# Optimization experiments

Hardware: AMD Instinct MI355X
Metric: run time of the kernel (lower is better)

## Reference

```python
import jax, jax.numpy as jnp
import numpy as np

HEADS = 8
NEG_SLOPE = 0.2  # PyG GATConv default LeakyReLU slope


def _gat_layer(x, src, dst, W, a_src, a_dst, bias, heads, out_ch):
    """PyG-style GATConv (concat heads, self-loops already appended, eval mode).
    x: [N, F_in]; src/dst: [E_tot] int; W: [F_in, heads*out_ch];
    a_src/a_dst: [heads, out_ch]; bias: [heads*out_ch].
    """
    N = x.shape[0]
    h = (x @ W).reshape(N, heads, out_ch)                      # [N, H, C]
    # per-node attention logits (gathered per edge as scalars, not features)
    al_s = jnp.einsum('nhc,hc->nh', h, a_src)                  # [N, H]
    al_d = jnp.einsum('nhc,hc->nh', h, a_dst)                  # [N, H]
    e = jax.nn.leaky_relu(al_s[src] + al_d[dst], negative_slope=NEG_SLOPE)  # [E, H]
    # segment softmax over incoming edges of each target node (stable)
    e_max = jax.ops.segment_max(e, dst, num_segments=N)        # self-loops => no empty segments
    ex = jnp.exp(e - e_max[dst])
    denom = jax.ops.segment_sum(ex, dst, num_segments=N)
    alpha = ex / (denom[dst] + 1e-16)                          # [E, H]
    # gather source features, weight, scatter-add to targets
    out = jax.ops.segment_sum(h[src] * alpha[:, :, None], dst, num_segments=N)  # [N, H, C]
    return out.reshape(N, heads * out_ch) + bias


def setup_inputs() -> dict:
    key = jax.random.key(0)
    ks = jax.random.split(key, 16)
    N, E, F_IN, NUM_CLASSES = 50000, 1600000, 128, 16
    s = 0.1
    return {
        'x': jax.random.normal(ks[0], (N, F_IN), dtype=jnp.float32),
        'edge_index': jax.random.randint(ks[1], (2, E), 0, N, dtype=jnp.int64),
        # GAT layer 1: 128 -> 8 heads x 8
        'W1': jax.random.normal(ks[2], (F_IN, 64), dtype=jnp.float32) * s,
        'a1_src': jax.random.normal(ks[3], (8, 8), dtype=jnp.float32) * s,
        'a1_dst': jax.random.normal(ks[4], (8, 8), dtype=jnp.float32) * s,
        'b1': jnp.zeros((64,), dtype=jnp.float32),
        # GAT layer 2: 64 -> 8 heads x 4
        'W2': jax.random.normal(ks[5], (64, 32), dtype=jnp.float32) * s,
        'a2_src': jax.random.normal(ks[6], (8, 4), dtype=jnp.float32) * s,
        'a2_dst': jax.random.normal(ks[7], (8, 4), dtype=jnp.float32) * s,
        'b2': jnp.zeros((32,), dtype=jnp.float32),
        # torch MultiheadAttention(32, 8): packed in_proj [96,32], out_proj [32,32]
        'in_proj_w': jax.random.normal(ks[8], (96, 32), dtype=jnp.float32) * s,
        'in_proj_b': jnp.zeros((96,), dtype=jnp.float32),
        'out_proj_w': jax.random.normal(ks[9], (32, 32), dtype=jnp.float32) * s,
        'out_proj_b': jnp.zeros((32,), dtype=jnp.float32),
        # fc: 32 -> num_classes
        'fc_w': jax.random.normal(ks[10], (NUM_CLASSES, 32), dtype=jnp.float32) * s,
        'fc_b': jnp.zeros((NUM_CLASSES,), dtype=jnp.float32),
    }


def reference(x, edge_index, W1, a1_src, a1_dst, b1, W2, a2_src, a2_dst, b2,
              in_proj_w, in_proj_b, out_proj_w, out_proj_b, fc_w, fc_b):
    N = x.shape[0]
    loops = jnp.arange(N, dtype=edge_index.dtype)
    src = jnp.concatenate([edge_index[0], loops])  # PyG add_self_loops=True
    dst = jnp.concatenate([edge_index[1], loops])

    h = jax.nn.elu(_gat_layer(x, src, dst, W1, a1_src, a1_dst, b1, HEADS, 8))   # [N, 64]
    h = jax.nn.elu(_gat_layer(h, src, dst, W2, a2_src, a2_dst, b2, HEADS, 4))   # [N, 32]

    # MultiheadAttention on h.unsqueeze(0): shape [1, N, 32] with torch's
    # seq-first layout => seq_len = 1, batch = N. Softmax over a single key
    # is identically 1 for every head, so out = out_proj(v_proj(h)).
    v = h @ in_proj_w[64:96].T + in_proj_b[64:96]   # v-projection slice of packed in_proj
    h = v @ out_proj_w.T + out_proj_b               # [N, 32]

    logits = h @ fc_w.T + fc_b                      # [N, num_classes]
    return jax.nn.log_softmax(logits, axis=1)
```

## Files before the change

### kernel.cpp

```cpp
#include <hip/hip_runtime.h>
#include <hip/hip_bf16.h>
#include <math.h>


#define BSHIFT 7
#define BMASK  ((1 << BSHIFT) - 1)
#define MAXNB  512
#define TILE   8192
#define XST    136
#define SMBYTES 36864
#define LESRC_MAX 6144

typedef __attribute__((ext_vector_type(8))) short short8;
typedef __attribute__((ext_vector_type(4))) float floatx4;
typedef __attribute__((ext_vector_type(2))) float floatx2;

__device__ __forceinline__ unsigned short f2bf(float f) {
    union { float f; unsigned int u; } v; v.f = f;
    unsigned int u = v.u;
    return (unsigned short)((u + 0x7FFFu + ((u >> 16) & 1u)) >> 16);
}
__device__ __forceinline__ float lrelu(float e) { return fmaxf(e, 0.2f * e); }
__device__ __forceinline__ float elu(float o) {
    return (o > 0.f) ? o : (__expf(o) - 1.f);
}

__global__ __launch_bounds__(256) void fused_pre_kernel(
    const float* __restrict__ x, const float* __restrict__ W,
    const float* __restrict__ a_src, const float* __restrict__ a_dst,
    char* __restrict__ rec1, float* __restrict__ ald, int N, int GB,
    const int* __restrict__ ei, int E, int Et, int NB, int CAP,
    int* __restrict__ gcount, unsigned int* __restrict__ rec, int NT,
    const float* __restrict__ in_proj_w, const float* __restrict__ in_proj_b,
    const float* __restrict__ out_proj_w, const float* __restrict__ out_proj_b,
    const float* __restrict__ fc_w, const float* __restrict__ fc_b,
    float* __restrict__ M, float* __restrict__ bf) {
    __shared__ __align__(16) char sm[SMBYTES];
    int t = threadIdx.x;
    int bid = blockIdx.x;
    if (bid < GB) {
        unsigned short* xs = (unsigned short*)sm;
        unsigned short* wt = xs + 64 * XST;
        int nb = bid * 64;
#pragma unroll
        for (int r = 0; r < 8; ++r) {
            int p = t + 256 * r;
            int row = p >> 5;
            int c4  = p & 31;
            int n = nb + row;
            float4 v = (n < N) ? ((const float4*)x)[(size_t)n * 32 + c4]
                               : make_float4(0.f, 0.f, 0.f, 0.f);
            unsigned short* dst = &xs[row * XST + c4 * 4];
            dst[0] = f2bf(v.x); dst[1] = f2bf(v.y);
            dst[2] = f2bf(v.z); dst[3] = f2bf(v.w);
        }
        {
            int n = t & 63, kg = t >> 6;
#pragma unroll
            for (int c = 0; c < 4; ++c) {
                int k0 = kg * 32 + c * 8;
                unsigned short* dst = &wt[n * XST + k0];
#pragma unroll
                for (int j = 0; j < 8; ++j)
                    dst[j] = f2bf(W[(k0 + j) * 64 + n]);
            }
        }
        __syncthreads();
        int wave = t >> 6, lane = t & 63;
        int m16 = lane & 15, quad = lane >> 4;
        floatx4 acc[4];
#pragma unroll
        for (int i = 0; i < 4; ++i) acc[i] = (floatx4){0.f, 0.f, 0.f, 0.f};
#pragma unroll
        for (int k = 0; k < 4; ++k) {
            int koff = k * 32 + quad * 8;
            short8 afrag = *(const short8*)&xs[(wave * 16 + m16) * XST + koff];
#pragma unroll
            for (int nt = 0; nt < 4; ++nt) {
                short8 bfrag = *(const short8*)&wt[(nt * 16 + m16) * XST + koff];
                acc[nt] = __builtin_amdgcn_mfma_f32_16x16x32_bf16(afrag, bfrag, acc[nt], 0, 0, 0);
            }
        }
        __syncthreads();
        float* hs = (float*)sm;
#pragma unroll
        for (int nt = 0; nt < 4; ++nt)
#pragma unroll
            for (int r = 0; r < 4; ++r)
                hs[(wave * 16 + quad * 4 + r) * 65 + nt * 16 + m16] = acc[nt][r];
        __syncthreads();
        float asv = a_src[lane], adv = a_dst[lane];
        for (int itn = 0; itn < 16; ++itn) {
            int nl = wave * 16 + itn;
            int n = nb + nl;
            if (n >= N) break;
            float v = hs[nl * 65 + lane];
            float ps = v * asv, pd = v * adv;
            ps += __shfl_xor(ps, 1); ps += __shfl_xor(ps, 2); ps += __shfl_xor(ps, 4);
            pd += __shfl_xor(pd, 1); pd += __shfl_xor(pd, 2); pd += __shfl_xor(pd, 4);
            if ((lane & 7) == 0) {
                *(float*)(rec1 + (size_t)n * 128 + 4 * (lane >> 3)) = ps;
                ald[n * 8 + (lane >> 3)] = pd;
            }
            if (lane < 16) {
                const float* hr = &hs[nl * 65 + lane * 4];
                int pk = __builtin_amdgcn_cvt_pk_fp8_f32(hr[0], hr[1], 0, false);
                pk = __builtin_amdgcn_cvt_pk_fp8_f32(hr[2], hr[3], pk, true);
                *(unsigned*)(rec1 + (size_t)n * 128 + 64 + 4 * lane) = (unsigned)pk;
            }
        }
    } else if (bid < GB + NT) {
        unsigned int* lrec = (unsigned int*)sm;
        int* h   = (int*)(sm + TILE * 4);
        int* cur = (int*)(sm + TILE * 4 + MAXNB * 4);
        for (int i = t; i < NB; i += 256) h[i] = 0;
        int tile0 = (bid - GB) * TILE;
        int cnt = Et - tile0; if (cnt > TILE) cnt = TILE;
        __syncthreads();
        for (int j = t; j < cnt; j += 256) {
            int jj = tile0 + j;
            int srcv, d;
            if (jj < E) { srcv = ei[jj]; d = ei[E + jj]; } else { srcv = jj - E; d = jj - E; }
            lrec[j] = (unsigned)srcv | ((unsigned)d << 16);
            atomicAdd(&h[d >> BSHIFT], 1);
        }
        __syncthreads();
        for (int i = t; i < NB; i += 256)
            cur[i] = h[i] ? atomicAdd(&gcount[i], h[i]) : 0;
        __syncthreads();
        for (int j = t; j < cnt; j += 256) {
            unsigned v = lrec[j];
            int b = v >> (16 + BSHIFT);
            int pos = atomicAdd(&cur[b], 1);
            if (pos < CAP)
                rec[(size_t)b * CAP + pos] =
                    (v & 0xFFFFu) | ((((v >> 16) & BMASK)) << 16);
        }
    } else {
        float* Wvo = (float*)sm;
        float* bvo = (float*)(sm + 4096);
        const float* Wv = in_proj_w + 64 * 32;
        const float* bv = in_proj_b + 64;
        for (int idx = t; idx < 1024; idx += 256) {
            int i = idx >> 5, j = idx & 31;
            float acc = 0.f;
            for (int k = 0; k < 32; ++k) acc += out_proj_w[i * 32 + k] * Wv[k * 32 + j];
            Wvo[idx] = acc;
        }
        if (t < 32) {
            float acc = 0.f;
            for (int k = 0; k < 32; ++k) acc += out_proj_w[t * 32 + k] * bv[k];
            bvo[t] = acc + out_proj_b[t];
        }
        __syncthreads();
        for (int idx = t; idx < 16 * 32; idx += 256) {
            int cc = idx >> 5, j = idx & 31;
            float acc = 0.f;
            for (int i = 0; i < 32; ++i) acc += fc_w[cc * 32 + i] * Wvo[i * 32 + j];
            M[idx] = acc;
        }
        if (t < 16) {
            float acc = 0.f;
            for (int i = 0; i < 32; ++i) acc += fc_w[t * 32 + i] * bvo[i];
            bf[t] = acc + fc_b[t];
        }
    }
}

__global__ __launch_bounds__(256) void csr_finalize_kernel(
    const unsigned int* __restrict__ rec, const int* __restrict__ gcount,
    int* __restrict__ rowp, unsigned short* __restrict__ esrc,
    int N, int Et, int CAP) {
    __shared__ int h[128];
    __shared__ int nb[128];
    __shared__ int cur[128];
    __shared__ int ssum[256];
    __shared__ unsigned short lesrc[LESRC_MAX];
    int b = blockIdx.x, t = threadIdx.x;
    size_t rbase = (size_t)b * CAP;
    int cnt = gcount[b]; if (cnt > CAP) cnt = CAP;
    if (t < 128) h[t] = 0;
    int acc = 0;
    for (int i = t; i < b; i += 256) {
        int v = gcount[i];
        acc += (v < CAP) ? v : CAP;
    }
    ssum[t] = acc;
    __syncthreads();
    for (int off = 128; off >= 1; off >>= 1) {
        if (t < off) ssum[t] += ssum[t + off];
        __syncthreads();
    }
    int obase = ssum[0];
    for (int i = t; i < cnt; i += 256)
        atomicAdd(&h[(rec[rbase + i] >> 16) & 127], 1);
    __syncthreads();
    if (t == 0) {
        int run = 0;
        for (int i = 0; i < 128; ++i) { nb[i] = run; run += h[i]; }
    }
    __syncthreads();
    if (t < 128) cur[t] = nb[t];
    int n0 = b << BSHIFT;
    if (t < 128 && n0 + t < N) rowp[n0 + t] = obase + nb[t];
    if (b == 0 && t == 0) rowp[N] = Et;
    __syncthreads();
    for (int i = t; i < cnt; i += 256) {
        unsigned r = rec[rbase + i];
        int pos = atomicAdd(&cur[(r >> 16) & 127], 1);
        lesrc[pos] = (unsigned short)(r & 0xFFFFu);
    }
    __syncthreads();
    for (int i = t; i < cnt; i += 256)
        esrc[obase + i] = lesrc[i];
}

__global__ __launch_bounds__(256) void gat_agg64_g2_kernel(
    const int* __restrict__ rowp, const unsigned short* __restrict__ esrc,
    const char* __restrict__ rec1, const float* __restrict__ ald_arr,
    const float* __restrict__ bias,
    const float* __restrict__ W2, const float* __restrict__ a2s,
    const float* __restrict__ a2d,
    char* __restrict__ rec2, float* __restrict__ ald2, int N) {
    __shared__ __align__(16) float W2p[2][8][32][4];
    __shared__ __align__(16) float oL[4][64];
    __shared__ __align__(16) float h2L[4][32];
    int t = threadIdx.x;
    for (int idx = t; idx < 2048; idx += 256) {
        int k = idx >> 5, l = idx & 31;
        W2p[k >> 5][(k & 31) >> 2][l][k & 3] = W2[idx];
    }
    __syncthreads();
    const int lane = t & 63;
    const int wv = t >> 6;
    const int e = lane >> 3;
    const int c = lane & 7;
    const int aoff = 4 * c;
    const int foff = 64 + 8 * c;
    int n = blockIdx.x * 4 + wv;
    if (n >= N) return;
    float aldv = ald_arr[n * 8 + c];
    int beg = rowp[n], end = rowp[n + 1];
    float dA = 0.f, dB = 0.f;
    floatx2 A0 = {0.f, 0.f}, A1 = {0.f, 0.f}, A2 = {0.f, 0.f}, A3 = {0.f, 0.f};
    floatx2 B0 = {0.f, 0.f}, B1 = {0.f, 0.f}, B2 = {0.f, 0.f}, B3 = {0.f, 0.f};
    int i = beg;
    for (; i + 32 <= end; i += 32) {
        int s0 = esrc[i + e],      s1 = esrc[i + 8 + e];
        int s2 = esrc[i + 16 + e], s3 = esrc[i + 24 + e];
        const char* r0 = rec1 + (size_t)s0 * 128;
        const char* r1 = rec1 + (size_t)s1 * 128;
        const char* r2 = rec1 + (size_t)s2 * 128;
        const char* r3 = rec1 + (size_t)s3 * 128;
        float e0 = *(const float*)(r0 + aoff), e1 = *(const float*)(r1 + aoff);
        float e2 = *(const float*)(r2 + aoff), e3 = *(const float*)(r3 + aoff);
        uint2 g0 = *(const uint2*)(r0 + foff), g1 = *(const uint2*)(r1 + foff);
        uint2 g2 = *(const uint2*)(r2 + foff), g3 = *(const uint2*)(r3 + foff);
        float w0 = __expf(lrelu(e0 + aldv));
        float w1 = __expf(lrelu(e1 + aldv));
        float w2 = __expf(lrelu(e2 + aldv));
        float w3 = __expf(lrelu(e3 + aldv));
        dA += w0 + w2; dB += w1 + w3;
        A0 += w0 * __builtin_amdgcn_cvt_pk_f32_fp8(g0.x, false);
        A1 += w0 * __builtin_amdgcn_cvt_pk_f32_fp8(g0.x, true);
        A2 += w0 * __builtin_amdgcn_cvt_pk_f32_fp8(g0.y, false);
        A3 += w0 * __builtin_amdgcn_cvt_pk_f32_fp8(g0.y, true);
        B0 += w1 * __builtin_amdgcn_cvt_pk_f32_fp8(g1.x, false);
        B1 += w1 * __builtin_amdgcn_cvt_pk_f32_fp8(g1.x, true);
        B2 += w1 * __builtin_amdgcn_cvt_pk_f32_fp8(g1.y, false);
        B3 += w1 * __builtin_amdgcn_cvt_pk_f32_fp8(g1.y, true);
        A0 += w2 * __builtin_amdgcn_cvt_pk_f32_fp8(g2.x, false);
        A1 += w2 * __builtin_amdgcn_cvt_pk_f32_fp8(g2.x, true);
        A2 += w2 * __builtin_amdgcn_cvt_pk_f32_fp8(g2.y, false);
        A3 += w2 * __builtin_amdgcn_cvt_pk_f32_fp8(g2.y, true);
        B0 += w3 * __builtin_amdgcn_cvt_pk_f32_fp8(g3.x, false);
        B1 += w3 * __builtin_amdgcn_cvt_pk_f32_fp8(g3.x, true);
        B2 += w3 * __builtin_amdgcn_cvt_pk_f32_fp8(g3.y, false);
        B3 += w3 * __builtin_amdgcn_cvt_pk_f32_fp8(g3.y, true);
    }
    for (; i < end; i += 32) {
        int i0 = i + e, i1 = i + 8 + e, i2 = i + 16 + e, i3 = i + 24 + e;
        bool v0 = i0 < end, v1 = i1 < end, v2 = i2 < end, v3 = i3 < end;
        int c0 = v0 ? i0 : beg;
        int c1 = v1 ? i1 : beg;
        int c2 = v2 ? i2 : beg;
        int c3 = v3 ? i3 : beg;
        int s0 = esrc[c0], s1 = esrc[c1], s2 = esrc[c2], s3 = esrc[c3];
        const char* r0 = rec1 + (size_t)s0 * 128;
        const char* r1 = rec1 + (size_t)s1 * 128;
        const char* r2 = rec1 + (size_t)s2 * 128;
        const char* r3 = rec1 + (size_t)s3 * 128;
        float e0 = *(const float*)(r0 + aoff), e1 = *(const float*)(r1 + aoff);
        float e2 = *(const float*)(r2 + aoff), e3 = *(const float*)(r3 + aoff);
        uint2 g0 = *(const uint2*)(r0 + foff), g1 = *(const uint2*)(r1 + foff);
        uint2 g2 = *(const uint2*)(r2 + foff), g3 = *(const uint2*)(r3 + foff);
        float w0 = v0 ? __expf(lrelu(e0 + aldv)) : 0.f;
        float w1 = v1 ? __expf(lrelu(e1 + aldv)) : 0.f;
        float w2 = v2 ? __expf(lrelu(e2 + aldv)) : 0.f;
        float w3 = v3 ? __expf(lrelu(e3 + aldv)) : 0.f;
        dA += w0 + w2; dB += w1 + w3;
        A0 += w0 * __builtin_amdgcn_cvt_pk_f32_fp8(g0.x, false);
        A1 += w0 * __builtin_amdgcn_cvt_pk_f32_fp8(g0.x, true);
        A2 += w0 * __builtin_amdgcn_cvt_pk_f32_fp8(g0.y, false);
        A3 += w0 * __builtin_amdgcn_cvt_pk_f32_fp8(g0.y, true);
        B0 += w1 * __builtin_amdgcn_cvt_pk_f32_fp8(g1.x, false);
        B1 += w1 * __builtin_amdgcn_cvt_pk_f32_fp8(g1.x, true);
        B2 += w1 * __builtin_amdgcn_cvt_pk_f32_fp8(g1.y, false);
        B3 += w1 * __builtin_amdgcn_cvt_pk_f32_fp8(g1.y, true);
        A0 += w2 * __builtin_amdgcn_cvt_pk_f32_fp8(g2.x, false);
        A1 += w2 * __builtin_amdgcn_cvt_pk_f32_fp8(g2.x, true);
        A2 += w2 * __builtin_amdgcn_cvt_pk_f32_fp8(g2.y, false);
        A3 += w2 * __builtin_amdgcn_cvt_pk_f32_fp8(g2.y, true);
        B0 += w3 * __builtin_amdgcn_cvt_pk_f32_fp8(g3.x, false);
        B1 += w3 * __builtin_amdgcn_cvt_pk_f32_fp8(g3.x, true);
        B2 += w3 * __builtin_amdgcn_cvt_pk_f32_fp8(g3.y, false);
        B3 += w3 * __builtin_amdgcn_cvt_pk_f32_fp8(g3.y, true);
    }
    float d = dA + dB;
    float P0 = A0.x + B0.x, P1 = A0.y + B0.y;
    float P2 = A1.x + B1.x, P3 = A1.y + B1.y;
    float P4 = A2.x + B2.x, P5 = A2.y + B2.y;
    float P6 = A3.x + B3.x, P7 = A3.y + B3.y;
    d  += __shfl_xor(d, 8);  d  += __shfl_xor(d, 16);  d  += __shfl_xor(d, 32);
    P0 += __shfl_xor(P0, 8); P0 += __shfl_xor(P0, 16); P0 += __shfl_xor(P0, 32);
    P1 += __shfl_xor(P1, 8); P1 += __shfl_xor(P1, 16); P1 += __shfl_xor(P1, 32);
    P2 += __shfl_xor(P2, 8); P2 += __shfl_xor(P2, 16); P2 += __shfl_xor(P2, 32);
    P3 += __shfl_xor(P3, 8); P3 += __shfl_xor(P3, 16); P3 += __shfl_xor(P3, 32);
    P4 += __shfl_xor(P4, 8); P4 += __shfl_xor(P4, 16); P4 += __shfl_xor(P4, 32);
    P5 += __shfl_xor(P5, 8); P5 += __shfl_xor(P5, 16); P5 += __shfl_xor(P5, 32);
    P6 += __shfl_xor(P6, 8); P6 += __shfl_xor(P6, 16); P6 += __shfl_xor(P6, 32);
    P7 += __shfl_xor(P7, 8); P7 += __shfl_xor(P7, 16); P7 += __shfl_xor(P7, 32);
    float inv = 1.f / (d + 1e-16f);
    float4 bv0 = ((const float4*)bias)[2 * c];
    float4 bv1 = ((const float4*)bias)[2 * c + 1];
    float o0 = elu(P0 * inv + bv0.x);
    float o1 = elu(P1 * inv + bv0.y);
    float o2 = elu(P2 * inv + bv0.z);
    float o3 = elu(P3 * inv + bv0.w);
    float o4 = elu(P4 * inv + bv1.x);
    float o5 = elu(P5 * inv + bv1.y);
    float o6 = elu(P6 * inv + bv1.z);
    float o7 = elu(P7 * inv + bv1.w);
    if (lane < 8) {
        *(float4*)&oL[wv][c * 8]     = make_float4(o0, o1, o2, o3);
        *(float4*)&oL[wv][c * 8 + 4] = make_float4(o4, o5, o6, o7);
    }
    const int l = lane & 31, kh = lane >> 5;
    const float* orow = &oL[wv][kh * 32];
    float a0 = 0.f, a1 = 0.f, a2 = 0.f, a3 = 0.f;
#pragma unroll
    for (int g = 0; g < 8; ++g) {
        float4 ov = *(const float4*)&orow[g * 4];
        float4 wv4 = *(const float4*)&W2p[kh][g][l][0];
        a0 += ov.x * wv4.x; a1 += ov.y * wv4.y;
        a2 += ov.z * wv4.z; a3 += ov.w * wv4.w;
    }
    float acc = (a0 + a1) + (a2 + a3);
    acc += __shfl_xor(acc, 32);
    float ps = acc * a2s[l], pd = acc * a2d[l];
    ps += __shfl_xor(ps, 1); ps += __shfl_xor(ps, 2);
    pd += __shfl_xor(pd, 1); pd += __shfl_xor(pd, 2);
    if (lane < 32) {
        h2L[wv][l] = acc;
        if ((l & 3) == 0) {
            *(float*)(rec2 + (size_t)n * 64 + 4 * (l >> 2)) = ps;
            ald2[n * 8 + (l >> 2)] = pd;
        }
    }
    if (lane < 8) {
        const float* hr = &h2L[wv][lane * 4];
        int pk = __builtin_amdgcn_cvt_pk_fp8_f32(hr[0], hr[1], 0, false);
        pk = __builtin_amdgcn_cvt_pk_fp8_f32(hr[2], hr[3], pk, true);
        *(unsigned*)(rec2 + (size_t)n * 64 + 32 + 4 * lane) = (unsigned)pk;
    }
}

__global__ __launch_bounds__(256) void gat_agg32_fin_kernel(
    const int* __restrict__ rowp, const unsigned short* __restrict__ esrc,
    const char* __restrict__ rec2, const float* __restrict__ ald_arr,
    const float* __restrict__ bias,
    const float* __restrict__ M, const float* __restrict__ bf,
    float* __restrict__ out, int N) {
    __shared__ __align__(16) float Mp[8][16][4];
    __shared__ float bfs[16];
    __shared__ __align__(16) float oL[4][32];
    int t = threadIdx.x;
    for (int i = t; i < 512; i += 256) {
        int j = i >> 5, k = i & 31;
        Mp[k >> 2][j][k & 3] = M[i];
    }
    if (t < 16) bfs[t] = bf[t];
    __syncthreads();
    const int lane = t & 63;
    const int wv = t >> 6;
    const int e = lane >> 3;
    const int c = lane & 7;
    const int aoff = 4 * c;
    const int foff = 32 + 4 * c;
    int n = blockIdx.x * 4 + wv;
    if (n >= N) return;
    float aldv = ald_arr[n * 8 + c];
    int beg = rowp[n], end = rowp[n + 1];
    float d0 = 0.f, d1 = 0.f, d2 = 0.f, d3 = 0.f;
    floatx2 p0a = {0.f, 0.f}, p0b = {0.f, 0.f};
    floatx2 p1a = {0.f, 0.f}, p1b = {0.f, 0.f};
    floatx2 p2a = {0.f, 0.f}, p2b = {0.f, 0.f};
    floatx2 p3a = {0.f, 0.f}, p3b = {0.f, 0.f};
    int base = beg;
    for (; base + 32 <= end; base += 32) {
        int s0 = esrc[base + e],      s1 = esrc[base + 8 + e];
        int s2 = esrc[base + 16 + e], s3 = esrc[base + 24 + e];
        const char* r0 = rec2 + (size_t)s0 * 64;
        const char* r1 = rec2 + (size_t)s1 * 64;
        const char* r2 = rec2 + (size_t)s2 * 64;
        const char* r3 = rec2 + (size_t)s3 * 64;
        float e0 = *(const float*)(r0 + aoff) + aldv;
        float e1 = *(const float*)(r1 + aoff) + aldv;
        float e2 = *(const float*)(r2 + aoff) + aldv;
        float e3 = *(const float*)(r3 + aoff) + aldv;
        unsigned g0 = *(const unsigned*)(r0 + foff);
        unsigned g1 = *(const unsigned*)(r1 + foff);
        unsigned g2 = *(const unsigned*)(r2 + foff);
        unsigned g3 = *(const unsigned*)(r3 + foff);
        float w0 = __expf(lrelu(e0));
        float w1 = __expf(lrelu(e1));
        float w2 = __expf(lrelu(e2));
        float w3 = __expf(lrelu(e3));
        d0 += w0; d1 += w1; d2 += w2; d3 += w3;
        p0a += w0 * __builtin_amdgcn_cvt_pk_f32_fp8(g0, false);
        p0b += w0 * __builtin_amdgcn_cvt_pk_f32_fp8(g0, true);
        p1a += w1 * __builtin_amdgcn_cvt_pk_f32_fp8(g1, false);
        p1b += w1 * __builtin_amdgcn_cvt_pk_f32_fp8(g1, true);
        p2a += w2 * __builtin_amdgcn_cvt_pk_f32_fp8(g2, false);
        p2b += w2 * __builtin_amdgcn_cvt_pk_f32_fp8(g2, true);
        p3a += w3 * __builtin_amdgcn_cvt_pk_f32_fp8(g3, false);
        p3b += w3 * __builtin_amdgcn_cvt_pk_f32_fp8(g3, true);
    }
    for (; base < end; base += 32) {
        int i0 = base + e;
        int i1 = base + 8 + e;
        int i2 = base + 16 + e;
        int i3 = base + 24 + e;
        bool v0 = i0 < end, v1 = i1 < end, v2 = i2 < end, v3 = i3 < end;
        int c0 = v0 ? i0 : beg;
        int c1 = v1 ? i1 : beg;
        int c2 = v2 ? i2 : beg;
        int c3 = v3 ? i3 : beg;
        int s0 = esrc[c0], s1 = esrc[c1], s2 = esrc[c2], s3 = esrc[c3];
        const char* r0 = rec2 + (size_t)s0 * 64;
        const char* r1 = rec2 + (size_t)s1 * 64;
        const char* r2 = rec2 + (size_t)s2 * 64;
        const char* r3 = rec2 + (size_t)s3 * 64;
        float e0 = *(const float*)(r0 + aoff) + aldv;
        float e1 = *(const float*)(r1 + aoff) + aldv;
        float e2 = *(const float*)(r2 + aoff) + aldv;
        float e3 = *(const float*)(r3 + aoff) + aldv;
        unsigned g0 = *(const unsigned*)(r0 + foff);
        unsigned g1 = *(const unsigned*)(r1 + foff);
        unsigned g2 = *(const unsigned*)(r2 + foff);
        unsigned g3 = *(const unsigned*)(r3 + foff);
        float w0 = v0 ? __expf(lrelu(e0)) : 0.f;
        float w1 = v1 ? __expf(lrelu(e1)) : 0.f;
        float w2 = v2 ? __expf(lrelu(e2)) : 0.f;
        float w3 = v3 ? __expf(lrelu(e3)) : 0.f;
        d0 += w0; d1 += w1; d2 += w2; d3 += w3;
        p0a += w0 * __builtin_amdgcn_cvt_pk_f32_fp8(g0, false);
        p0b += w0 * __builtin_amdgcn_cvt_pk_f32_fp8(g0, true);
        p1a += w1 * __builtin_amdgcn_cvt_pk_f32_fp8(g1, false);
        p1b += w1 * __builtin_amdgcn_cvt_pk_f32_fp8(g1, true);
        p2a += w2 * __builtin_amdgcn_cvt_pk_f32_fp8(g2, false);
        p2b += w2 * __builtin_amdgcn_cvt_pk_f32_fp8(g2, true);
        p3a += w3 * __builtin_amdgcn_cvt_pk_f32_fp8(g3, false);
        p3b += w3 * __builtin_amdgcn_cvt_pk_f32_fp8(g3, true);
    }
    float d = (d0 + d1) + (d2 + d3);
    floatx2 Pa = (p0a + p1a) + (p2a + p3a);
    floatx2 Pb = (p0b + p1b) + (p2b + p3b);
    float P0 = Pa.x, P1 = Pa.y, P2 = Pb.x, P3 = Pb.y;
    d  += __shfl_xor(d, 8);  d  += __shfl_xor(d, 16);  d  += __shfl_xor(d, 32);
    P0 += __shfl_xor(P0, 8); P0 += __shfl_xor(P0, 16); P0 += __shfl_xor(P0, 32);
    P1 += __shfl_xor(P1, 8); P1 += __shfl_xor(P1, 16); P1 += __shfl_xor(P1, 32);
    P2 += __shfl_xor(P2, 8); P2 += __shfl_xor(P2, 16); P2 += __shfl_xor(P2, 32);
    P3 += __shfl_xor(P3, 8); P3 += __shfl_xor(P3, 16); P3 += __shfl_xor(P3, 32);
    float inv = 1.f / (d + 1e-16f);
    float4 bv = ((const float4*)bias)[c];
    float o0 = elu(P0 * inv + bv.x);
    float o1 = elu(P1 * inv + bv.y);
    float o2 = elu(P2 * inv + bv.z);
    float o3 = elu(P3 * inv + bv.w);
    if (lane < 8) *(float4*)&oL[wv][c * 4] = make_float4(o0, o1, o2, o3);
    const int j = lane & 15;
    const float* orow = oL[wv];
    float a0 = 0.f, a1 = 0.f, a2 = 0.f, a3 = 0.f;
#pragma unroll
    for (int g = 0; g < 8; ++g) {
        float4 ov = *(const float4*)&orow[g * 4];
        float4 mv = *(const float4*)&Mp[g][j][0];
        a0 += ov.x * mv.x; a1 += ov.y * mv.y;
        a2 += ov.z * mv.z; a3 += ov.w * mv.w;
    }
    float logit = (a0 + a1) + (a2 + a3) + bfs[j];
    float mx = logit;
    mx = fmaxf(mx, __shfl_xor(mx, 1));
    mx = fmaxf(mx, __shfl_xor(mx, 2));
    mx = fmaxf(mx, __shfl_xor(mx, 4));
    mx = fmaxf(mx, __shfl_xor(mx, 8));
    float ex = __expf(logit - mx);
    float se = ex;
    se += __shfl_xor(se, 1);
    se += __shfl_xor(se, 2);
    se += __shfl_xor(se, 4);
    se += __shfl_xor(se, 8);
    float res = logit - (mx + __logf(se));
    if (lane < 16) out[(size_t)n * 16 + j] = res;
}

extern "C" void kernel_launch(void* const* d_in, const int* in_sizes, int n_in,
                              void* d_out, int out_size, void* d_ws, size_t ws_size,
                              hipStream_t stream) {
    const float* x   = (const float*)d_in[0];
    const int*   ei  = (const int*)d_in[1];
    const float* W1  = (const float*)d_in[2];
    const float* a1s = (const float*)d_in[3];
    const float* a1d = (const float*)d_in[4];
    const float* b1  = (const float*)d_in[5];
    const float* W2  = (const float*)d_in[6];
    const float* a2s = (const float*)d_in[7];
    const float* a2d = (const float*)d_in[8];
    const float* b2  = (const float*)d_in[9];
    const float* ipw = (const float*)d_in[10];
    const float* ipb = (const float*)d_in[11];
    const float* opw = (const float*)d_in[12];
    const float* opb = (const float*)d_in[13];
    const float* fcw = (const float*)d_in[14];
    const float* fcb = (const float*)d_in[15];
    float* out = (float*)d_out;

    int N = in_sizes[0] / 128;
    int E = in_sizes[1] / 2;
    int Et = E + N;
    int NB = (N + BMASK) >> BSHIFT;
    int NTILES = (Et + TILE - 1) / TILE;
    int GB = (N + 63) / 64;
    int CAP = Et / NB;
    CAP = CAP + CAP / 8 + 256;
    CAP = (CAP + 255) & ~255;
    if (CAP > LESRC_MAX) CAP = LESRC_MAX;

    char* ws = (char*)d_ws;
    size_t off = 0;
    auto alloc = [&](size_t bytes) -> void* {
        void* p = ws + off;
        off += bytes;
        off = (off + 255) & ~(size_t)255;
        return p;
    };
    int*   bcount = (int*)alloc(MAXNB * 4);
    unsigned int*   rec  = (unsigned int*)alloc((size_t)NB * CAP * 4);
    int*   rowp   = (int*)alloc((size_t)(N + 1) * 4);
    unsigned short* esrc = (unsigned short*)alloc((size_t)Et * 2);
    char* rec1   = (char*)alloc((size_t)N * 128);
    float* al1d  = (float*)alloc((size_t)N * 8 * 4);
    char* rec2   = (char*)alloc((size_t)N * 64);
    float* al2d  = (float*)alloc((size_t)N * 8 * 4);
    float* Mf    = (float*)alloc(512 * 4);
    float* bff   = (float*)alloc(16 * 4);
    (void)ws_size; (void)n_in; (void)out_size;

    hipMemsetAsync(bcount, 0, MAXNB * 4, stream);
    fused_pre_kernel<<<GB + NTILES + 1, 256, 0, stream>>>(
        x, W1, a1s, a1d, rec1, al1d, N, GB,
        ei, E, Et, NB, CAP, bcount, rec, NTILES,
        ipw, ipb, opw, opb, fcw, fcb, Mf, bff);
    csr_finalize_kernel<<<NB, 256, 0, stream>>>(rec, bcount, rowp, esrc, N, Et, CAP);

    gat_agg64_g2_kernel<<<(N + 3) / 4, 256, 0, stream>>>(
        rowp, esrc, rec1, al1d, b1, W2, a2s, a2d, rec2, al2d, N);
    gat_agg32_fin_kernel<<<(N + 3) / 4, 256, 0, stream>>>(
        rowp, esrc, rec2, al2d, b2, Mf, bff, out, N);
}
```

Baseline: 212.3 us.

## Compact gather records with fp16 logits, add low-degree fast path, precompute bf16 W

```diff
diff --git a/kernel.cpp b/kernel.cpp
--- a/kernel.cpp
+++ b/kernel.cpp
@@ -1,5 +1,6 @@
 #include <hip/hip_runtime.h>
 #include <hip/hip_bf16.h>
+#include <hip/hip_fp16.h>
 #include <math.h>
 
 
@@ -25,8 +26,18 @@
     return (o > 0.f) ? o : (__expf(o) - 1.f);
 }
 
+__global__ __launch_bounds__(256) void prep_kernel(
+    const float* __restrict__ W, unsigned short* __restrict__ wtb,
+    int* __restrict__ gcount) {
+    int t = threadIdx.x;
+    if (blockIdx.x == 0) { gcount[t] = 0; gcount[t + 256] = 0; }
+    int idx = blockIdx.x * 256 + t;
+    int n = idx >> 7, k = idx & 127;
+    wtb[idx] = f2bf(W[k * 64 + n]);
+}
+
 __global__ __launch_bounds__(256) void fused_pre_kernel(
-    const float* __restrict__ x, const float* __restrict__ W,
+    const float* __restrict__ x, const unsigned short* __restrict__ wtb,
     const float* __restrict__ a_src, const float* __restrict__ a_dst,
     char* __restrict__ rec1, float* __restrict__ ald, int N, int GB,
     const int* __restrict__ ei, int E, int Et, int NB, int CAP,
@@ -59,10 +70,7 @@
 #pragma unroll
             for (int c = 0; c < 4; ++c) {
                 int k0 = kg * 32 + c * 8;
-                unsigned short* dst = &wt[n * XST + k0];
-#pragma unroll
-                for (int j = 0; j < 8; ++j)
-                    dst[j] = f2bf(W[(k0 + j) * 64 + n]);
+                *(short8*)&wt[n * XST + k0] = *(const short8*)&wtb[n * 128 + k0];
             }
         }
         __syncthreads();
@@ -98,15 +106,20 @@
             float ps = v * asv, pd = v * adv;
             ps += __shfl_xor(ps, 1); ps += __shfl_xor(ps, 2); ps += __shfl_xor(ps, 4);
             pd += __shfl_xor(pd, 1); pd += __shfl_xor(pd, 2); pd += __shfl_xor(pd, 4);
-            if ((lane & 7) == 0) {
-                *(float*)(rec1 + (size_t)n * 128 + 4 * (lane >> 3)) = ps;
+            float av = __shfl(ps, (lane & 7) * 8);
+            if ((lane & 7) == 0)
                 ald[n * 8 + (lane >> 3)] = pd;
-            }
-            if (lane < 16) {
-                const float* hr = &hs[nl * 65 + lane * 4];
-                int pk = __builtin_amdgcn_cvt_pk_fp8_f32(hr[0], hr[1], 0, false);
-                pk = __builtin_amdgcn_cvt_pk_fp8_f32(hr[2], hr[3], pk, true);
-                *(unsigned*)(rec1 + (size_t)n * 128 + 64 + 4 * lane) = (unsigned)pk;
+            if (lane < 8) {
+                const float* hr = &hs[nl * 65 + lane * 8];
+                int pk0 = __builtin_amdgcn_cvt_pk_fp8_f32(hr[0], hr[1], 0, false);
+                pk0 = __builtin_amdgcn_cvt_pk_fp8_f32(hr[2], hr[3], pk0, true);
+                int pk1 = __builtin_amdgcn_cvt_pk_fp8_f32(hr[4], hr[5], 0, false);
+                pk1 = __builtin_amdgcn_cvt_pk_fp8_f32(hr[6], hr[7], pk1, true);
+                *(__half*)(rec1 + (size_t)n * 80 + 2 * lane) = __float2half(av);
+                uint2 w2v;
+                w2v.x = (unsigned)pk0;
+                w2v.y = (unsigned)pk1;
+                *(uint2*)(rec1 + (size_t)n * 80 + 16 + 8 * lane) = w2v;
             }
         }
     } else if (bid < GB + NT) {
@@ -226,125 +239,172 @@
     __shared__ __align__(16) float oL[4][64];
     __shared__ __align__(16) float h2L[4][32];
     int t = threadIdx.x;
-    for (int idx = t; idx < 2048; idx += 256) {
-        int k = idx >> 5, l = idx & 31;
-        W2p[k >> 5][(k & 31) >> 2][l][k & 3] = W2[idx];
-    }
-    __syncthreads();
     const int lane = t & 63;
     const int wv = t >> 6;
     const int e = lane >> 3;
     const int c = lane & 7;
-    const int aoff = 4 * c;
-    const int foff = 64 + 8 * c;
+    const int aoff = 2 * c;
+    const int foff = 16 + 8 * c;
     int n = blockIdx.x * 4 + wv;
-    if (n >= N) return;
-    float aldv = ald_arr[n * 8 + c];
-    int beg = rowp[n], end = rowp[n + 1];
-    float dA = 0.f, dB = 0.f;
-    floatx2 A0 = {0.f, 0.f}, A1 = {0.f, 0.f}, A2 = {0.f, 0.f}, A3 = {0.f, 0.f};
-    floatx2 B0 = {0.f, 0.f}, B1 = {0.f, 0.f}, B2 = {0.f, 0.f}, B3 = {0.f, 0.f};
-    int i = beg;
-    for (; i + 32 <= end; i += 32) {
-        int s0 = esrc[i + e],      s1 = esrc[i + 8 + e];
-        int s2 = esrc[i + 16 + e], s3 = esrc[i + 24 + e];
-        const char* r0 = rec1 + (size_t)s0 * 128;
-        const char* r1 = rec1 + (size_t)s1 * 128;
-        const char* r2 = rec1 + (size_t)s2 * 128;
-        const char* r3 = rec1 + (size_t)s3 * 128;
-        float e0 = *(const float*)(r0 + aoff), e1 = *(const float*)(r1 + aoff);
-        float e2 = *(const float*)(r2 + aoff), e3 = *(const float*)(r3 + aoff);
-        uint2 g0 = *(const uint2*)(r0 + foff), g1 = *(const uint2*)(r1 + foff);
-        uint2 g2 = *(const uint2*)(r2 + foff), g3 = *(const uint2*)(r3 + foff);
-        float w0 = __expf(lrelu(e0 + aldv));
-        float w1 = __expf(lrelu(e1 + aldv));
-        float w2 = __expf(lrelu(e2 + aldv));
-        float w3 = __expf(lrelu(e3 + aldv));
-        dA += w0 + w2; dB += w1 + w3;
-        A0 += w0 * __builtin_amdgcn_cvt_pk_f32_fp8(g0.x, false);
-        A1 += w0 * __builtin_amdgcn_cvt_pk_f32_fp8(g0.x, true);
-        A2 += w0 * __builtin_amdgcn_cvt_pk_f32_fp8(g0.y, false);
-        A3 += w0 * __builtin_amdgcn_cvt_pk_f32_fp8(g0.y, true);
-        B0 += w1 * __builtin_amdgcn_cvt_pk_f32_fp8(g1.x, false);
-        B1 += w1 * __builtin_amdgcn_cvt_pk_f32_fp8(g1.x, true);
-        B2 += w1 * __builtin_amdgcn_cvt_pk_f32_fp8(g1.y, false);
-        B3 += w1 * __builtin_amdgcn_cvt_pk_f32_fp8(g1.y, true);
-        A0 += w2 * __builtin_amdgcn_cvt_pk_f32_fp8(g2.x, false);
-        A1 += w2 * __builtin_amdgcn_cvt_pk_f32_fp8(g2.x, true);
-        A2 += w2 * __builtin_amdgcn_cvt_pk_f32_fp8(g2.y, false);
-        A3 += w2 * __builtin_amdgcn_cvt_pk_f32_fp8(g2.y, true);
-        B0 += w3 * __builtin_amdgcn_cvt_pk_f32_fp8(g3.x, false);
-        B1 += w3 * __builtin_amdgcn_cvt_pk_f32_fp8(g3.x, true);
-        B2 += w3 * __builtin_amdgcn_cvt_pk_f32_fp8(g3.y, false);
-        B3 += w3 * __builtin_amdgcn_cvt_pk_f32_fp8(g3.y, true);
-    }
-    for (; i < end; i += 32) {
-        int i0 = i + e, i1 = i + 8 + e, i2 = i + 16 + e, i3 = i + 24 + e;
-        bool v0 = i0 < end, v1 = i1 < end, v2 = i2 < end, v3 = i3 < end;
-        int c0 = v0 ? i0 : beg;
-        int c1 = v1 ? i1 : beg;
-        int c2 = v2 ? i2 : beg;
-        int c3 = v3 ? i3 : beg;
-        int s0 = esrc[c0], s1 = esrc[c1], s2 = esrc[c2], s3 = esrc[c3];
-        const char* r0 = rec1 + (size_t)s0 * 128;
-        const char* r1 = rec1 + (size_t)s1 * 128;
-        const char* r2 = rec1 + (size_t)s2 * 128;
-        const char* r3 = rec1 + (size_t)s3 * 128;
-        float e0 = *(const float*)(r0 + aoff), e1 = *(const float*)(r1 + aoff);
-        float e2 = *(const float*)(r2 + aoff), e3 = *(const float*)(r3 + aoff);
-        uint2 g0 = *(const uint2*)(r0 + foff), g1 = *(const uint2*)(r1 + foff);
-        uint2 g2 = *(const uint2*)(r2 + foff), g3 = *(const uint2*)(r3 + foff);
-        float w0 = v0 ? __expf(lrelu(e0 + aldv)) : 0.f;
-        float w1 = v1 ? __expf(lrelu(e1 + aldv)) : 0.f;
-        float w2 = v2 ? __expf(lrelu(e2 + aldv)) : 0.f;
-        float w3 = v3 ? __expf(lrelu(e3 + aldv)) : 0.f;
-        dA += w0 + w2; dB += w1 + w3;
-        A0 += w0 * __builtin_amdgcn_cvt_pk_f32_fp8(g0.x, false);
-        A1 += w0 * __builtin_amdgcn_cvt_pk_f32_fp8(g0.x, true);
-        A2 += w0 * __builtin_amdgcn_cvt_pk_f32_fp8(g0.y, false);
-        A3 += w0 * __builtin_amdgcn_cvt_pk_f32_fp8(g0.y, true);
-        B0 += w1 * __builtin_amdgcn_cvt_pk_f32_fp8(g1.x, false);
-        B1 += w1 * __builtin_amdgcn_cvt_pk_f32_fp8(g1.x, true);
-        B2 += w1 * __builtin_amdgcn_cvt_pk_f32_fp8(g1.y, false);
-        B3 += w1 * __builtin_amdgcn_cvt_pk_f32_fp8(g1.y, true);
-        A0 += w2 * __builtin_amdgcn_cvt_pk_f32_fp8(g2.x, false);
-        A1 += w2 * __builtin_amdgcn_cvt_pk_f32_fp8(g2.x, true);
-        A2 += w2 * __builtin_amdgcn_cvt_pk_f32_fp8(g2.y, false);
-        A3 += w2 * __builtin_amdgcn_cvt_pk_f32_fp8(g2.y, true);
-        B0 += w3 * __builtin_amdgcn_cvt_pk_f32_fp8(g3.x, false);
-        B1 += w3 * __builtin_amdgcn_cvt_pk_f32_fp8(g3.x, true);
-        B2 += w3 * __builtin_amdgcn_cvt_pk_f32_fp8(g3.y, false);
-        B3 += w3 * __builtin_amdgcn_cvt_pk_f32_fp8(g3.y, true);
-    }
-    float d = dA + dB;
-    float P0 = A0.x + B0.x, P1 = A0.y + B0.y;
-    float P2 = A1.x + B1.x, P3 = A1.y + B1.y;
-    float P4 = A2.x + B2.x, P5 = A2.y + B2.y;
-    float P6 = A3.x + B3.x, P7 = A3.y + B3.y;
-    d  += __shfl_xor(d, 8);  d  += __shfl_xor(d, 16);  d  += __shfl_xor(d, 32);
-    P0 += __shfl_xor(P0, 8); P0 += __shfl_xor(P0, 16); P0 += __shfl_xor(P0, 32);
-    P1 += __shfl_xor(P1, 8); P1 += __shfl_xor(P1, 16); P1 += __shfl_xor(P1, 32);
-    P2 += __shfl_xor(P2, 8); P2 += __shfl_xor(P2, 16); P2 += __shfl_xor(P2, 32);
-    P3 += __shfl_xor(P3, 8); P3 += __shfl_xor(P3, 16); P3 += __shfl_xor(P3, 32);
-    P4 += __shfl_xor(P4, 8); P4 += __shfl_xor(P4, 16); P4 += __shfl_xor(P4, 32);
-    P5 += __shfl_xor(P5, 8); P5 += __shfl_xor(P5, 16); P5 += __shfl_xor(P5, 32);
-    P6 += __shfl_xor(P6, 8); P6 += __shfl_xor(P6, 16); P6 += __shfl_xor(P6, 32);
-    P7 += __shfl_xor(P7, 8); P7 += __shfl_xor(P7, 16); P7 += __shfl_xor(P7, 32);
-    float inv = 1.f / (d + 1e-16f);
-    float4 bv0 = ((const float4*)bias)[2 * c];
-    float4 bv1 = ((const float4*)bias)[2 * c + 1];
-    float o0 = elu(P0 * inv + bv0.x);
-    float o1 = elu(P1 * inv + bv0.y);
-    float o2 = elu(P2 * inv + bv0.z);
-    float o3 = elu(P3 * inv + bv0.w);
-    float o4 = elu(P4 * inv + bv1.x);
-    float o5 = elu(P5 * inv + bv1.y);
-    float o6 = elu(P6 * inv + bv1.z);
-    float o7 = elu(P7 * inv + bv1.w);
-    if (lane < 8) {
-        *(float4*)&oL[wv][c * 8]     = make_float4(o0, o1, o2, o3);
-        *(float4*)&oL[wv][c * 8 + 4] = make_float4(o4, o5, o6, o7);
-    }
+    bool active = n < N;
+    if (active) {
+        float aldv = ald_arr[n * 8 + c];
+        int beg = rowp[n], end = rowp[n + 1];
+        int deg = end - beg;
+        float dA = 0.f, dB = 0.f;
+        floatx2 A0 = {0.f, 0.f}, A1 = {0.f, 0.f}, A2 = {0.f, 0.f}, A3 = {0.f, 0.f};
+        floatx2 B0 = {0.f, 0.f}, B1 = {0.f, 0.f}, B2 = {0.f, 0.f}, B3 = {0.f, 0.f};
+        if (deg <= 48) {
+            int s[6];
+#pragma unroll
+            for (int g = 0; g < 6; ++g) {
+                int p = beg + g * 8 + e;
+                s[g] = esrc[(p < end) ? p : beg];
+            }
+            float ev[6];
+            uint2 gg[6];
+#pragma unroll
+            for (int g = 0; g < 6; ++g) {
+                const char* r = rec1 + (size_t)s[g] * 80;
+                ev[g] = __half2float(*(const __half*)(r + aoff));
+                gg[g] = *(const uint2*)(r + foff);
+            }
+#pragma unroll
+            for (int g = 0; g < 6; ++g) {
+                bool vv = (beg + g * 8 + e) < end;
+                float w = vv ? __expf(lrelu(ev[g] + aldv)) : 0.f;
+                if ((g & 1) == 0) {
+                    dA += w;
+                    A0 += w * __builtin_amdgcn_cvt_pk_f32_fp8(gg[g].x, false);
+                    A1 += w * __builtin_amdgcn_cvt_pk_f32_fp8(gg[g].x, true);
+                    A2 += w * __builtin_amdgcn_cvt_pk_f32_fp8(gg[g].y, false);
+                    A3 += w * __builtin_amdgcn_cvt_pk_f32_fp8(gg[g].y, true);
+                } else {
+                    dB += w;
+                    B0 += w * __builtin_amdgcn_cvt_pk_f32_fp8(gg[g].x, false);
+                    B1 += w * __builtin_amdgcn_cvt_pk_f32_fp8(gg[g].x, true);
+                    B2 += w * __builtin_amdgcn_cvt_pk_f32_fp8(gg[g].y, false);
+                    B3 += w * __builtin_amdgcn_cvt_pk_f32_fp8(gg[g].y, true);
+                }
+            }
+        } else {
+            int i = beg;
+            for (; i + 32 <= end; i += 32) {
+                int s0 = esrc[i + e],      s1 = esrc[i + 8 + e];
+                int s2 = esrc[i + 16 + e], s3 = esrc[i + 24 + e];
+                const char* r0 = rec1 + (size_t)s0 * 80;
+                const char* r1 = rec1 + (size_t)s1 * 80;
+                const char* r2 = rec1 + (size_t)s2 * 80;
+                const char* r3 = rec1 + (size_t)s3 * 80;
+                float e0 = __half2float(*(const __half*)(r0 + aoff));
+                float e1 = __half2float(*(const __half*)(r1 + aoff));
+                float e2 = __half2float(*(const __half*)(r2 + aoff));
+                float e3 = __half2float(*(const __half*)(r3 + aoff));
+                uint2 g0 = *(const uint2*)(r0 + foff);
+                uint2 g1 = *(const uint2*)(r1 + foff);
+                uint2 g2 = *(const uint2*)(r2 + foff);
+                uint2 g3 = *(const uint2*)(r3 + foff);
+                float w0 = __expf(lrelu(e0 + aldv));
+                float w1 = __expf(lrelu(e1 + aldv));
+                float w2 = __expf(lrelu(e2 + aldv));
+                float w3 = __expf(lrelu(e3 + aldv));
+                dA += w0 + w2; dB += w1 + w3;
+                A0 += w0 * __builtin_amdgcn_cvt_pk_f32_fp8(g0.x, false);
+                A1 += w0 * __builtin_amdgcn_cvt_pk_f32_fp8(g0.x, true);
+                A2 += w0 * __builtin_amdgcn_cvt_pk_f32_fp8(g0.y, false);
+                A3 += w0 * __builtin_amdgcn_cvt_pk_f32_fp8(g0.y, true);
+                B0 += w1 * __builtin_amdgcn_cvt_pk_f32_fp8(g1.x, false);
+                B1 += w1 * __builtin_amdgcn_cvt_pk_f32_fp8(g1.x, true);
+                B2 += w1 * __builtin_amdgcn_cvt_pk_f32_fp8(g1.y, false);
+                B3 += w1 * __builtin_amdgcn_cvt_pk_f32_fp8(g1.y, true);
+                A0 += w2 * __builtin_amdgcn_cvt_pk_f32_fp8(g2.x, false);
+                A1 += w2 * __builtin_amdgcn_cvt_pk_f32_fp8(g2.x, true);
+                A2 += w2 * __builtin_amdgcn_cvt_pk_f32_fp8(g2.y, false);
+                A3 += w2 * __builtin_amdgcn_cvt_pk_f32_fp8(g2.y, true);
+                B0 += w3 * __builtin_amdgcn_cvt_pk_f32_fp8(g3.x, false);
+                B1 += w3 * __builtin_amdgcn_cvt_pk_f32_fp8(g3.x, true);
+                B2 += w3 * __builtin_amdgcn_cvt_pk_f32_fp8(g3.y, false);
+                B3 += w3 * __builtin_amdgcn_cvt_pk_f32_fp8(g3.y, true);
+            }
+            for (; i < end; i += 32) {
+                int i0 = i + e, i1 = i + 8 + e, i2 = i + 16 + e, i3 = i + 24 + e;
+                bool v0 = i0 < end, v1 = i1 < end, v2 = i2 < end, v3 = i3 < end;
+                int c0 = v0 ? i0 : beg;
+                int c1 = v1 ? i1 : beg;
+                int c2 = v2 ? i2 : beg;
+                int c3 = v3 ? i3 : beg;
+                int s0 = esrc[c0], s1 = esrc[c1], s2 = esrc[c2], s3 = esrc[c3];
+                const char* r0 = rec1 + (size_t)s0 * 80;
+                const char* r1 = rec1 + (size_t)s1 * 80;
+                const char* r2 = rec1 + (size_t)s2 * 80;
+                const char* r3 = rec1 + (size_t)s3 * 80;
+                float e0 = __half2float(*(const __half*)(r0 + aoff));
+                float e1 = __half2float(*(const __half*)(r1 + aoff));
+                float e2 = __half2float(*(const __half*)(r2 + aoff));
+                float e3 = __half2float(*(const __half*)(r3 + aoff));
+                uint2 g0 = *(const uint2*)(r0 + foff);
+                uint2 g1 = *(const uint2*)(r1 + foff);
+                uint2 g2 = *(const uint2*)(r2 + foff);
+                uint2 g3 = *(const uint2*)(r3 + foff);
+                float w0 = v0 ? __expf(lrelu(e0 + aldv)) : 0.f;
+                float w1 = v1 ? __expf(lrelu(e1 + aldv)) : 0.f;
+                float w2 = v2 ? __expf(lrelu(e2 + aldv)) : 0.f;
+                float w3 = v3 ? __expf(lrelu(e3 + aldv)) : 0.f;
+                dA += w0 + w2; dB += w1 + w3;
+                A0 += w0 * __builtin_amdgcn_cvt_pk_f32_fp8(g0.x, false);
+                A1 += w0 * __builtin_amdgcn_cvt_pk_f32_fp8(g0.x, true);
+                A2 += w0 * __builtin_amdgcn_cvt_pk_f32_fp8(g0.y, false);
+                A3 += w0 * __builtin_amdgcn_cvt_pk_f32_fp8(g0.y, true);
+                B0 += w1 * __builtin_amdgcn_cvt_pk_f32_fp8(g1.x, false);
+                B1 += w1 * __builtin_amdgcn_cvt_pk_f32_fp8(g1.x, true);
+                B2 += w1 * __builtin_amdgcn_cvt_pk_f32_fp8(g1.y, false);
+                B3 += w1 * __builtin_amdgcn_cvt_pk_f32_fp8(g1.y, true);
+                A0 += w2 * __builtin_amdgcn_cvt_pk_f32_fp8(g2.x, false);
+                A1 += w2 * __builtin_amdgcn_cvt_pk_f32_fp8(g2.x, true);
+                A2 += w2 * __builtin_amdgcn_cvt_pk_f32_fp8(g2.y, false);
+                A3 += w2 * __builtin_amdgcn_cvt_pk_f32_fp8(g2.y, true);
+                B0 += w3 * __builtin_amdgcn_cvt_pk_f32_fp8(g3.x, false);
+                B1 += w3 * __builtin_amdgcn_cvt_pk_f32_fp8(g3.x, true);
+                B2 += w3 * __builtin_amdgcn_cvt_pk_f32_fp8(g3.y, false);
+                B3 += w3 * __builtin_amdgcn_cvt_pk_f32_fp8(g3.y, true);
+            }
+        }
+        float d = dA + dB;
+        float P0 = A0.x + B0.x, P1 = A0.y + B0.y;
+        float P2 = A1.x + B1.x, P3 = A1.y + B1.y;
+        float P4 = A2.x + B2.x, P5 = A2.y + B2.y;
+        float P6 = A3.x + B3.x, P7 = A3.y + B3.y;
+        d  += __shfl_xor(d, 8);  d  += __shfl_xor(d, 16);  d  += __shfl_xor(d, 32);
+        P0 += __shfl_xor(P0, 8); P0 += __shfl_xor(P0, 16); P0 += __shfl_xor(P0, 32);
+        P1 += __shfl_xor(P1, 8); P1 += __shfl_xor(P1, 16); P1 += __shfl_xor(P1, 32);
+        P2 += __shfl_xor(P2, 8); P2 += __shfl_xor(P2, 16); P2 += __shfl_xor(P2, 32);
+        P3 += __shfl_xor(P3, 8); P3 += __shfl_xor(P3, 16); P3 += __shfl_xor(P3, 32);
+        P4 += __shfl_xor(P4, 8); P4 += __shfl_xor(P4, 16); P4 += __shfl_xor(P4, 32);
+        P5 += __shfl_xor(P5, 8); P5 += __shfl_xor(P5, 16); P5 += __shfl_xor(P5, 32);
+        P6 += __shfl_xor(P6, 8); P6 += __shfl_xor(P6, 16); P6 += __shfl_xor(P6, 32);
+        P7 += __shfl_xor(P7, 8); P7 += __shfl_xor(P7, 16); P7 += __shfl_xor(P7, 32);
+        float inv = 1.f / (d + 1e-16f);
+        float4 bv0 = ((const float4*)bias)[2 * c];
+        float4 bv1 = ((const float4*)bias)[2 * c + 1];
+        float o0 = elu(P0 * inv + bv0.x);
+        float o1 = elu(P1 * inv + bv0.y);
+        float o2 = elu(P2 * inv + bv0.z);
+        float o3 = elu(P3 * inv + bv0.w);
+        float o4 = elu(P4 * inv + bv1.x);
+        float o5 = elu(P5 * inv + bv1.y);
+        float o6 = elu(P6 * inv + bv1.z);
+        float o7 = elu(P7 * inv + bv1.w);
+        if (lane < 8) {
+            *(float4*)&oL[wv][c * 8]     = make_float4(o0, o1, o2, o3);
+            *(float4*)&oL[wv][c * 8 + 4] = make_float4(o4, o5, o6, o7);
+        }
+    }
+    for (int idx = t; idx < 2048; idx += 256) {
+        int k = idx >> 5, l = idx & 31;
+        W2p[k >> 5][(k & 31) >> 2][l][k & 3] = W2[idx];
+    }
+    __syncthreads();
+    if (!active) return;
     const int l = lane & 31, kh = lane >> 5;
     const float* orow = &oL[wv][kh * 32];
     float a0 = 0.f, a1 = 0.f, a2 = 0.f, a3 = 0.f;
@@ -360,18 +420,17 @@
     float ps = acc * a2s[l], pd = acc * a2d[l];
     ps += __shfl_xor(ps, 1); ps += __shfl_xor(ps, 2);
     pd += __shfl_xor(pd, 1); pd += __shfl_xor(pd, 2);
+    float psv = __shfl(ps, (lane & 7) * 4);
     if (lane < 32) {
         h2L[wv][l] = acc;
-        if ((l & 3) == 0) {
-            *(float*)(rec2 + (size_t)n * 64 + 4 * (l >> 2)) = ps;
-            ald2[n * 8 + (l >> 2)] = pd;
-        }
+        if ((l & 3) == 0) ald2[n * 8 + (l >> 2)] = pd;
     }
     if (lane < 8) {
         const float* hr = &h2L[wv][lane * 4];
         int pk = __builtin_amdgcn_cvt_pk_fp8_f32(hr[0], hr[1], 0, false);
         pk = __builtin_amdgcn_cvt_pk_fp8_f32(hr[2], hr[3], pk, true);
-        *(unsigned*)(rec2 + (size_t)n * 64 + 32 + 4 * lane) = (unsigned)pk;
+        *(__half*)(rec2 + (size_t)n * 48 + 2 * lane) = __float2half(psv);
+        *(unsigned*)(rec2 + (size_t)n * 48 + 16 + 4 * lane) = (unsigned)pk;
     }
 }
 
@@ -385,110 +444,153 @@
     __shared__ float bfs[16];
     __shared__ __align__(16) float oL[4][32];
     int t = threadIdx.x;
-    for (int i = t; i < 512; i += 256) {
-        int j = i >> 5, k = i & 31;
-        Mp[k >> 2][j][k & 3] = M[i];
-    }
-    if (t < 16) bfs[t] = bf[t];
-    __syncthreads();
     const int lane = t & 63;
     const int wv = t >> 6;
     const int e = lane >> 3;
     const int c = lane & 7;
-    const int aoff = 4 * c;
-    const int foff = 32 + 4 * c;
+    const int aoff = 2 * c;
+    const int foff = 16 + 4 * c;
     int n = blockIdx.x * 4 + wv;
-    if (n >= N) return;
-    float aldv = ald_arr[n * 8 + c];
-    int beg = rowp[n], end = rowp[n + 1];
-    float d0 = 0.f, d1 = 0.f, d2 = 0.f, d3 = 0.f;
-    floatx2 p0a = {0.f, 0.f}, p0b = {0.f, 0.f};
-    floatx2 p1a = {0.f, 0.f}, p1b = {0.f, 0.f};
-    floatx2 p2a = {0.f, 0.f}, p2b = {0.f, 0.f};
-    floatx2 p3a = {0.f, 0.f}, p3b = {0.f, 0.f};
-    int base = beg;
-    for (; base + 32 <= end; base += 32) {
-        int s0 = esrc[base + e],      s1 = esrc[base + 8 + e];
-        int s2 = esrc[base + 16 + e], s3 = esrc[base + 24 + e];
-        const char* r0 = rec2 + (size_t)s0 * 64;
-        const char* r1 = rec2 + (size_t)s1 * 64;
-        const char* r2 = rec2 + (size_t)s2 * 64;
-        const char* r3 = rec2 + (size_t)s3 * 64;
-        float e0 = *(const float*)(r0 + aoff) + aldv;
-        float e1 = *(const float*)(r1 + aoff) + aldv;
-        float e2 = *(const float*)(r2 + aoff) + aldv;
-        float e3 = *(const float*)(r3 + aoff) + aldv;
-        unsigned g0 = *(const unsigned*)(r0 + foff);
-        unsigned g1 = *(const unsigned*)(r1 + foff);
-        unsigned g2 = *(const unsigned*)(r2 + foff);
-        unsigned g3 = *(const unsigned*)(r3 + foff);
-        float w0 = __expf(lrelu(e0));
-        float w1 = __expf(lrelu(e1));
-        float w2 = __expf(lrelu(e2));
-        float w3 = __expf(lrelu(e3));
-        d0 += w0; d1 += w1; d2 += w2; d3 += w3;
-        p0a += w0 * __builtin_amdgcn_cvt_pk_f32_fp8(g0, false);
-        p0b += w0 * __builtin_amdgcn_cvt_pk_f32_fp8(g0, true);
-        p1a += w1 * __builtin_amdgcn_cvt_pk_f32_fp8(g1, false);
-        p1b += w1 * __builtin_amdgcn_cvt_pk_f32_fp8(g1, true);
-        p2a += w2 * __builtin_amdgcn_cvt_pk_f32_fp8(g2, false);
-        p2b += w2 * __builtin_amdgcn_cvt_pk_f32_fp8(g2, true);
-        p3a += w3 * __builtin_amdgcn_cvt_pk_f32_fp8(g3, false);
-        p3b += w3 * __builtin_amdgcn_cvt_pk_f32_fp8(g3, true);
-    }
-    for (; base < end; base += 32) {
-        int i0 = base + e;
-        int i1 = base + 8 + e;
-        int i2 = base + 16 + e;
-        int i3 = base + 24 + e;
-        bool v0 = i0 < end, v1 = i1 < end, v2 = i2 < end, v3 = i3 < end;
-        int c0 = v0 ? i0 : beg;
-        int c1 = v1 ? i1 : beg;
-        int c2 = v2 ? i2 : beg;
-        int c3 = v3 ? i3 : beg;
-        int s0 = esrc[c0], s1 = esrc[c1], s2 = esrc[c2], s3 = esrc[c3];
-        const char* r0 = rec2 + (size_t)s0 * 64;
-        const char* r1 = rec2 + (size_t)s1 * 64;
-        const char* r2 = rec2 + (size_t)s2 * 64;
-        const char* r3 = rec2 + (size_t)s3 * 64;
-        float e0 = *(const float*)(r0 + aoff) + aldv;
-        float e1 = *(const float*)(r1 + aoff) + aldv;
-        float e2 = *(const float*)(r2 + aoff) + aldv;
-        float e3 = *(const float*)(r3 + aoff) + aldv;
-        unsigned g0 = *(const unsigned*)(r0 + foff);
-        unsigned g1 = *(const unsigned*)(r1 + foff);
-        unsigned g2 = *(const unsigned*)(r2 + foff);
-        unsigned g3 = *(const unsigned*)(r3 + foff);
-        float w0 = v0 ? __expf(lrelu(e0)) : 0.f;
-        float w1 = v1 ? __expf(lrelu(e1)) : 0.f;
-        float w2 = v2 ? __expf(lrelu(e2)) : 0.f;
-        float w3 = v3 ? __expf(lrelu(e3)) : 0.f;
-        d0 += w0; d1 += w1; d2 += w2; d3 += w3;
-        p0a += w0 * __builtin_amdgcn_cvt_pk_f32_fp8(g0, false);
-        p0b += w0 * __builtin_amdgcn_cvt_pk_f32_fp8(g0, true);
-        p1a += w1 * __builtin_amdgcn_cvt_pk_f32_fp8(g1, false);
-        p1b += w1 * __builtin_amdgcn_cvt_pk_f32_fp8(g1, true);
-        p2a += w2 * __builtin_amdgcn_cvt_pk_f32_fp8(g2, false);
-        p2b += w2 * __builtin_amdgcn_cvt_pk_f32_fp8(g2, true);
-        p3a += w3 * __builtin_amdgcn_cvt_pk_f32_fp8(g3, false);
-        p3b += w3 * __builtin_amdgcn_cvt_pk_f32_fp8(g3, true);
-    }
-    float d = (d0 + d1) + (d2 + d3);
-    floatx2 Pa = (p0a + p1a) + (p2a + p3a);
-    floatx2 Pb = (p0b + p1b) + (p2b + p3b);
-    float P0 = Pa.x, P1 = Pa.y, P2 = Pb.x, P3 = Pb.y;
-    d  += __shfl_xor(d, 8);  d  += __shfl_xor(d, 16);  d  += __shfl_xor(d, 32);
-    P0 += __shfl_xor(P0, 8); P0 += __shfl_xor(P0, 16); P0 += __shfl_xor(P0, 32);
-    P1 += __shfl_xor(P1, 8); P1 += __shfl_xor(P1, 16); P1 += __shfl_xor(P1, 32);
-    P2 += __shfl_xor(P2, 8); P2 += __shfl_xor(P2, 16); P2 += __shfl_xor(P2, 32);
-    P3 += __shfl_xor(P3, 8); P3 += __shfl_xor(P3, 16); P3 += __shfl_xor(P3, 32);
-    float inv = 1.f / (d + 1e-16f);
-    float4 bv = ((const float4*)bias)[c];
-    float o0 = elu(P0 * inv + bv.x);
-    float o1 = elu(P1 * inv + bv.y);
-    float o2 = elu(P2 * inv + bv.z);
-    float o3 = elu(P3 * inv + bv.w);
-    if (lane < 8) *(float4*)&oL[wv][c * 4] = make_float4(o0, o1, o2, o3);
+    bool active = n < N;
+    if (active) {
+        float aldv = ald_arr[n * 8 + c];
+        int beg = rowp[n], end = rowp[n + 1];
+        int deg = end - beg;
+        float d0 = 0.f, d1 = 0.f, d2 = 0.f, d3 = 0.f;
+        floatx2 p0a = {0.f, 0.f}, p0b = {0.f, 0.f};
+        floatx2 p1a = {0.f, 0.f}, p1b = {0.f, 0.f};
+        floatx2 p2a = {0.f, 0.f}, p2b = {0.f, 0.f};
+        floatx2 p3a = {0.f, 0.f}, p3b = {0.f, 0.f};
+        if (deg <= 64) {
+            int s[8];
+#pragma unroll
+            for (int g = 0; g < 8; ++g) {
+                int p = beg + g * 8 + e;
+                s[g] = esrc[(p < end) ? p : beg];
+            }
+            float ev[8];
+            unsigned gg[8];
+#pragma unroll
+            for (int g = 0; g < 8; ++g) {
+                const char* r = rec2 + (size_t)s[g] * 48;
+                ev[g] = __half2float(*(const __half*)(r + aoff));
+                gg[g] = *(const unsigned*)(r + foff);
+            }
+#pragma unroll
+            for (int g = 0; g < 8; ++g) {
+                bool vv = (beg + g * 8 + e) < end;
+                float w = vv ? __expf(lrelu(ev[g] + aldv)) : 0.f;
+                if ((g & 3) == 0) {
+                    d0 += w;
+                    p0a += w * __builtin_amdgcn_cvt_pk_f32_fp8(gg[g], false);
+                    p0b += w * __builtin_amdgcn_cvt_pk_f32_fp8(gg[g], true);
+                } else if ((g & 3) == 1) {
+                    d1 += w;
+                    p1a += w * __builtin_amdgcn_cvt_pk_f32_fp8(gg[g], false);
+                    p1b += w * __builtin_amdgcn_cvt_pk_f32_fp8(gg[g], true);
+                } else if ((g & 3) == 2) {
+                    d2 += w;
+                    p2a += w * __builtin_amdgcn_cvt_pk_f32_fp8(gg[g], false);
+                    p2b += w * __builtin_amdgcn_cvt_pk_f32_fp8(gg[g], true);
+                } else {
+                    d3 += w;
+                    p3a += w * __builtin_amdgcn_cvt_pk_f32_fp8(gg[g], false);
+                    p3b += w * __builtin_amdgcn_cvt_pk_f32_fp8(gg[g], true);
+                }
+            }
+        } else {
+            int base = beg;
+            for (; base + 32 <= end; base += 32) {
+                int s0 = esrc[base + e],      s1 = esrc[base + 8 + e];
+                int s2 = esrc[base + 16 + e], s3 = esrc[base + 24 + e];
+                const char* r0 = rec2 + (size_t)s0 * 48;
+                const char* r1 = rec2 + (size_t)s1 * 48;
+                const char* r2 = rec2 + (size_t)s2 * 48;
+                const char* r3 = rec2 + (size_t)s3 * 48;
+                float e0 = __half2float(*(const __half*)(r0 + aoff)) + aldv;
+                float e1 = __half2float(*(const __half*)(r1 + aoff)) + aldv;
+                float e2 = __half2float(*(const __half*)(r2 + aoff)) + aldv;
+                float e3 = __half2float(*(const __half*)(r3 + aoff)) + aldv;
+                unsigned g0 = *(const unsigned*)(r0 + foff);
+                unsigned g1 = *(const unsigned*)(r1 + foff);
+                unsigned g2 = *(const unsigned*)(r2 + foff);
+                unsigned g3 = *(const unsigned*)(r3 + foff);
+                float w0 = __expf(lrelu(e0));
+                float w1 = __expf(lrelu(e1));
+                float w2 = __expf(lrelu(e2));
+                float w3 = __expf(lrelu(e3));
+                d0 += w0; d1 += w1; d2 += w2; d3 += w3;
+                p0a += w0 * __builtin_amdgcn_cvt_pk_f32_fp8(g0, false);
+                p0b += w0 * __builtin_amdgcn_cvt_pk_f32_fp8(g0, true);
+                p1a += w1 * __builtin_amdgcn_cvt_pk_f32_fp8(g1, false);
+                p1b += w1 * __builtin_amdgcn_cvt_pk_f32_fp8(g1, true);
+                p2a += w2 * __builtin_amdgcn_cvt_pk_f32_fp8(g2, false);
+                p2b += w2 * __builtin_amdgcn_cvt_pk_f32_fp8(g2, true);
+                p3a += w3 * __builtin_amdgcn_cvt_pk_f32_fp8(g3, false);
+                p3b += w3 * __builtin_amdgcn_cvt_pk_f32_fp8(g3, true);
+            }
+            for (; base < end; base += 32) {
+                int i0 = base + e;
+                int i1 = base + 8 + e;
+                int i2 = base + 16 + e;
+                int i3 = base + 24 + e;
+                bool v0 = i0 < end, v1 = i1 < end, v2 = i2 < end, v3 = i3 < end;
+                int c0 = v0 ? i0 : beg;
+                int c1 = v1 ? i1 : beg;
+                int c2 = v2 ? i2 : beg;
+                int c3 = v3 ? i3 : beg;
+                int s0 = esrc[c0], s1 = esrc[c1], s2 = esrc[c2], s3 = esrc[c3];
+                const char* r0 = rec2 + (size_t)s0 * 48;
+                const char* r1 = rec2 + (size_t)s1 * 48;
+                const char* r2 = rec2 + (size_t)s2 * 48;
+                const char* r3 = rec2 + (size_t)s3 * 48;
+                float e0 = __half2float(*(const __half*)(r0 + aoff)) + aldv;
+                float e1 = __half2float(*(const __half*)(r1 + aoff)) + aldv;
+                float e2 = __half2float(*(const __half*)(r2 + aoff)) + aldv;
+                float e3 = __half2float(*(const __half*)(r3 + aoff)) + aldv;
+                unsigned g0 = *(const unsigned*)(r0 + foff);
+                unsigned g1 = *(const unsigned*)(r1 + foff);
+                unsigned g2 = *(const unsigned*)(r2 + foff);
+                unsigned g3 = *(const unsigned*)(r3 + foff);
+                float w0 = v0 ? __expf(lrelu(e0)) : 0.f;
+                float w1 = v1 ? __expf(lrelu(e1)) : 0.f;
+                float w2 = v2 ? __expf(lrelu(e2)) : 0.f;
+                float w3 = v3 ? __expf(lrelu(e3)) : 0.f;
+                d0 += w0; d1 += w1; d2 += w2; d3 += w3;
+                p0a += w0 * __builtin_amdgcn_cvt_pk_f32_fp8(g0, false);
+                p0b += w0 * __builtin_amdgcn_cvt_pk_f32_fp8(g0, true);
+                p1a += w1 * __builtin_amdgcn_cvt_pk_f32_fp8(g1, false);
+                p1b += w1 * __builtin_amdgcn_cvt_pk_f32_fp8(g1, true);
+                p2a += w2 * __builtin_amdgcn_cvt_pk_f32_fp8(g2, false);
+                p2b += w2 * __builtin_amdgcn_cvt_pk_f32_fp8(g2, true);
+                p3a += w3 * __builtin_amdgcn_cvt_pk_f32_fp8(g3, false);
+                p3b += w3 * __builtin_amdgcn_cvt_pk_f32_fp8(g3, true);
+            }
+        }
+        float d = (d0 + d1) + (d2 + d3);
+        floatx2 Pa = (p0a + p1a) + (p2a + p3a);
+        floatx2 Pb = (p0b + p1b) + (p2b + p3b);
+        float P0 = Pa.x, P1 = Pa.y, P2 = Pb.x, P3 = Pb.y;
+        d  += __shfl_xor(d, 8);  d  += __shfl_xor(d, 16);  d  += __shfl_xor(d, 32);
+        P0 += __shfl_xor(P0, 8); P0 += __shfl_xor(P0, 16); P0 += __shfl_xor(P0, 32);
+        P1 += __shfl_xor(P1, 8); P1 += __shfl_xor(P1, 16); P1 += __shfl_xor(P1, 32);
+        P2 += __shfl_xor(P2, 8); P2 += __shfl_xor(P2, 16); P2 += __shfl_xor(P2, 32);
+        P3 += __shfl_xor(P3, 8); P3 += __shfl_xor(P3, 16); P3 += __shfl_xor(P3, 32);
+        float inv = 1.f / (d + 1e-16f);
+        float4 bv = ((const float4*)bias)[c];
+        float o0 = elu(P0 * inv + bv.x);
+        float o1 = elu(P1 * inv + bv.y);
+        float o2 = elu(P2 * inv + bv.z);
+        float o3 = elu(P3 * inv + bv.w);
+        if (lane < 8) *(float4*)&oL[wv][c * 4] = make_float4(o0, o1, o2, o3);
+    }
+    for (int i = t; i < 512; i += 256) {
+        int j = i >> 5, k = i & 31;
+        Mp[k >> 2][j][k & 3] = M[i];
+    }
+    if (t < 16) bfs[t] = bf[t];
+    __syncthreads();
+    if (!active) return;
     const int j = lane & 15;
     const float* orow = oL[wv];
     float a0 = 0.f, a1 = 0.f, a2 = 0.f, a3 = 0.f;
@@ -559,17 +661,18 @@
     unsigned int*   rec  = (unsigned int*)alloc((size_t)NB * CAP * 4);
     int*   rowp   = (int*)alloc((size_t)(N + 1) * 4);
     unsigned short* esrc = (unsigned short*)alloc((size_t)Et * 2);
-    char* rec1   = (char*)alloc((size_t)N * 128);
+    char* rec1   = (char*)alloc((size_t)N * 80);
     float* al1d  = (float*)alloc((size_t)N * 8 * 4);
-    char* rec2   = (char*)alloc((size_t)N * 64);
+    char* rec2   = (char*)alloc((size_t)N * 48);
     float* al2d  = (float*)alloc((size_t)N * 8 * 4);
     float* Mf    = (float*)alloc(512 * 4);
     float* bff   = (float*)alloc(16 * 4);
+    unsigned short* wtb = (unsigned short*)alloc(64 * 128 * 2);
     (void)ws_size; (void)n_in; (void)out_size;
 
-    hipMemsetAsync(bcount, 0, MAXNB * 4, stream);
+    prep_kernel<<<32, 256, 0, stream>>>(W1, wtb, bcount);
     fused_pre_kernel<<<GB + NTILES + 1, 256, 0, stream>>>(
-        x, W1, a1s, a1d, rec1, al1d, N, GB,
+        x, wtb, a1s, a1d, rec1, al1d, N, GB,
         ei, E, Et, NB, CAP, bcount, rec, NTILES,
         ipw, ipb, opw, opb, fcw, fcb, Mf, bff);
     csr_finalize_kernel<<<NB, 256, 0, stream>>>(rec, bcount, rowp, esrc, N, Et, CAP);
```

Result: faster. 207.1 us (-2.4%).
